# Performance work log

Hardware: AMD Instinct MI355X
Metric: run time of the kernel (lower is better)

Reference implementation:

```python
import jax, jax.numpy as jnp
import numpy as np

B = 8192
N_CLASSES = 1024
MARGIN = 0.1
THRESH = 0.5
SCALE_POS = 2.0
SCALE_NEG = 40.0
EPS = 1e-5


def setup_inputs() -> dict:
    key = jax.random.key(0)
    k1, k2 = jax.random.split(key)
    # cosine-similarity-like values in [-1, 1]
    sim_mat = jax.random.uniform(k1, (B, B), dtype=jnp.float32, minval=-1.0, maxval=1.0)
    labels = jax.random.randint(k2, (B,), 0, N_CLASSES, dtype=jnp.int64)
    return {"sim_mat": sim_mat, "labels": labels}


def reference(sim_mat, labels):
    # [B, B] pair masks
    same = labels[:, None] == labels[None, :]
    pos_mask = same & (sim_mat < 1.0 - EPS)        # positives, excluding self-sim ~ 1
    neg_mask = ~same

    # per-row hardest positive (min) / hardest negative (max); inf sentinels when empty
    min_pos = jnp.min(jnp.where(pos_mask, sim_mat, jnp.inf), axis=1)   # [B]
    max_neg = jnp.max(jnp.where(neg_mask, sim_mat, -jnp.inf), axis=1)  # [B]

    # pair mining: keep informative pairs only
    sel_neg = neg_mask & (sim_mat + MARGIN > min_pos[:, None])
    sel_pos = pos_mask & (sim_mat - MARGIN < max_neg[:, None])

    valid = jnp.any(sel_neg, axis=1) & jnp.any(sel_pos, axis=1)  # rows contributing to loss

    # masked soft-plus style logsumexp losses (sim bounded in [-1,1], exp is safe)
    pos_sum = jnp.sum(jnp.where(sel_pos, jnp.exp(-SCALE_POS * (sim_mat - THRESH)), 0.0), axis=1)
    neg_sum = jnp.sum(jnp.where(sel_neg, jnp.exp(SCALE_NEG * (sim_mat - THRESH)), 0.0), axis=1)
    pos_loss = jnp.log1p(pos_sum) / SCALE_POS
    neg_loss = jnp.log1p(neg_sum) / SCALE_NEG

    loss = jnp.sum(jnp.where(valid, pos_loss + neg_loss, 0.0)) / sim_mat.shape[0]
    return loss
```

## Files before the change

### kernel.cpp

```cpp
#include <hip/hip_runtime.h>
#include <math.h>

namespace {
constexpr int   kB        = 8192;
constexpr int   kBlock    = 256;
constexpr int   kVec      = 4;
constexpr int   kChunks   = kB / (kBlock * kVec);
constexpr float kMargin   = 0.1f;
constexpr float kThresh   = 0.5f;
constexpr float kScalePos = 2.0f;
constexpr float kScaleNeg = 40.0f;
constexpr float kEps      = 1e-5f;
}

__global__ __launch_bounds__(kBlock, 6) void ms_loss_kernel(
    const float* __restrict__ sim,
    const int*   __restrict__ labels,
    float*       __restrict__ ws,
    float*       __restrict__ out)
{
  const int tid  = threadIdx.x;
  const int wave = tid >> 6;
  const int lane = tid & 63;
  const int row  = blockIdx.x;

  const float* __restrict__ srow = sim + (size_t)row * kB;
  float4 v[kChunks];
  #pragma unroll
  for (int k = 0; k < kChunks; ++k)
    v[k] = *reinterpret_cast<const float4*>(srow + k * (kBlock * kVec) + tid * kVec);

  const int ml = labels[row];
  unsigned int m = 0u;
  #pragma unroll
  for (int k = 0; k < kChunks; k += 2) {
    const int4 la = *reinterpret_cast<const int4*>(labels + (k + 0) * (kBlock * kVec) + tid * kVec);
    const int4 lb = *reinterpret_cast<const int4*>(labels + (k + 1) * (kBlock * kVec) + tid * kVec);
    m |= (unsigned)(la.x == ml) << ((k + 0) * 4 + 0);
    m |= (unsigned)(la.y == ml) << ((k + 0) * 4 + 1);
    m |= (unsigned)(la.z == ml) << ((k + 0) * 4 + 2);
    m |= (unsigned)(la.w == ml) << ((k + 0) * 4 + 3);
    m |= (unsigned)(lb.x == ml) << ((k + 1) * 4 + 0);
    m |= (unsigned)(lb.y == ml) << ((k + 1) * 4 + 1);
    m |= (unsigned)(lb.z == ml) << ((k + 1) * 4 + 2);
    m |= (unsigned)(lb.w == ml) << ((k + 1) * 4 + 3);
  }

  #pragma unroll
  for (int k = 0; k < kChunks; ++k)
    asm volatile("" : "+v"(v[k].x), "+v"(v[k].y), "+v"(v[k].z), "+v"(v[k].w));

  __shared__ float s_min[kBlock / 64];
  __shared__ float s_max[kBlock / 64];
  __shared__ float s_pos[kBlock / 64];
  __shared__ float s_neg[kBlock / 64];

  float min_pos =  INFINITY;
  float max_neg = -INFINITY;
  #pragma unroll
  for (int k = 0; k < kChunks; ++k) {
    const float4 f = v[k];
    const float xs[4] = {f.x, f.y, f.z, f.w};
    #pragma unroll
    for (int c = 0; c < 4; ++c) {
      const bool  same = (m >> (k * 4 + c)) & 1u;
      const float x = xs[c];
      min_pos = fminf(min_pos, (same && x < 1.0f - kEps) ? x : INFINITY);
      max_neg = fmaxf(max_neg, same ? -INFINITY : x);
    }
  }
  #pragma unroll
  for (int off = 32; off > 0; off >>= 1) {
    min_pos = fminf(min_pos, __shfl_xor(min_pos, off, 64));
    max_neg = fmaxf(max_neg, __shfl_xor(max_neg, off, 64));
  }
  if (lane == 0) { s_min[wave] = min_pos; s_max[wave] = max_neg; }
  __syncthreads();
  min_pos = fminf(fminf(s_min[0], s_min[1]), fminf(s_min[2], s_min[3]));
  max_neg = fmaxf(fmaxf(s_max[0], s_max[1]), fmaxf(s_max[2], s_max[3]));

  float pos_sum = 0.0f, neg_sum = 0.0f;
  #pragma unroll
  for (int k = 0; k < kChunks; ++k) {
    const float4 f = v[k];
    const float xs[4] = {f.x, f.y, f.z, f.w};
    #pragma unroll
    for (int c = 0; c < 4; ++c) {
      const bool  same = (m >> (k * 4 + c)) & 1u;
      const float x = xs[c];
      const float a = same ? -kScalePos : kScaleNeg;
      const float e = __expf(a * (x - kThresh));
      const bool selp = same && (x < 1.0f - kEps) && (x - kMargin < max_neg);
      const bool seln = (!same) && (x + kMargin > min_pos);
      pos_sum += selp ? e : 0.0f;
      neg_sum += seln ? e : 0.0f;
    }
  }
  #pragma unroll
  for (int off = 32; off > 0; off >>= 1) {
    pos_sum += __shfl_xor(pos_sum, off, 64);
    neg_sum += __shfl_xor(neg_sum, off, 64);
  }
  if (lane == 0) { s_pos[wave] = pos_sum; s_neg[wave] = neg_sum; }
  __syncthreads();
  if (tid == 0) {
    pos_sum = (s_pos[0] + s_pos[1]) + (s_pos[2] + s_pos[3]);
    neg_sum = (s_neg[0] + s_neg[1]) + (s_neg[2] + s_neg[3]);
    const bool  valid    = (pos_sum > 0.0f) && (neg_sum > 0.0f);
    const float row_loss = valid ? (log1pf(pos_sum) * (1.0f / kScalePos)
                                  + log1pf(neg_sum) * (1.0f / kScaleNeg))
                                 : 0.0f;
    if (ws) {
      ws[row] = row_loss;
    } else if (row_loss != 0.0f) {
      atomicAdd(out, row_loss * (1.0f / (float)kB));
    }
  }
}

__global__ __launch_bounds__(256) void ms_reduce_kernel(
    const float* __restrict__ ws,
    float*       __restrict__ out)
{
  const int tid = threadIdx.x;
  float s = 0.0f;
  #pragma unroll
  for (int k = 0; k < 8; ++k) {
    const float4 f = *reinterpret_cast<const float4*>(ws + k * 1024 + tid * 4);
    s += (f.x + f.y) + (f.z + f.w);
  }
  #pragma unroll
  for (int off = 32; off > 0; off >>= 1)
    s += __shfl_xor(s, off, 64);
  __shared__ float sm[4];
  if ((tid & 63) == 0) sm[tid >> 6] = s;
  __syncthreads();
  if (tid == 0)
    out[0] = ((sm[0] + sm[1]) + (sm[2] + sm[3])) * (1.0f / (float)kB);
}

extern "C" void kernel_launch(void* const* d_in, const int* in_sizes, int n_in,
                              void* d_out, int out_size, void* d_ws, size_t ws_size,
                              hipStream_t stream) {
  const float* sim    = (const float*)d_in[0];
  const int*   labels = (const int*)d_in[1];
  float*       out    = (float*)d_out;

  hipMemsetAsync(d_out, 0, sizeof(float) * (size_t)out_size, stream);

  if (d_ws != nullptr && ws_size >= (size_t)kB * sizeof(float)) {
    float* ws = (float*)d_ws;
    ms_loss_kernel<<<dim3(kB), dim3(kBlock), 0, stream>>>(sim, labels, ws, out);
    ms_reduce_kernel<<<dim3(1), dim3(256), 0, stream>>>(ws, out);
  } else {
    ms_loss_kernel<<<dim3(kB), dim3(kBlock), 0, stream>>>(sim, labels, nullptr, out);
  }
}
```

Baseline: 355.6 us.

## Process eight rows per block with double-buffered prefetch of next row

Each block now handles eight consecutive rows instead of one, with a 1024-block grid. It loads labels once per block, packed as 16-bit pairs, and reuses them across rows. While one row is being computed, the next row's data is prefetched into a second register buffer. This amortises label loads and launch overhead and hides memory latency behind compute. The cost is more registers (launch bounds lowered to 4 blocks per SM), extra barriers per row, and labels truncated to 16 bits, which is only correct for fewer than 65536 classes.

```diff
diff --git a/kernel.cpp b/kernel.cpp
--- a/kernel.cpp
+++ b/kernel.cpp
@@ -4,8 +4,8 @@
 namespace {
 constexpr int   kB        = 8192;
 constexpr int   kBlock    = 256;
-constexpr int   kVec      = 4;
-constexpr int   kChunks   = kB / (kBlock * kVec);
+constexpr int   kRows     = 8;
+constexpr int   kGrid     = kB / kRows;
 constexpr float kMargin   = 0.1f;
 constexpr float kThresh   = 0.5f;
 constexpr float kScalePos = 2.0f;
@@ -13,7 +13,7 @@
 constexpr float kEps      = 1e-5f;
 }
 
-__global__ __launch_bounds__(kBlock, 6) void ms_loss_kernel(
+__global__ __launch_bounds__(kBlock, 4) void ms_loss_kernel(
     const float* __restrict__ sim,
     const int*   __restrict__ labels,
     float*       __restrict__ ws,
@@ -22,100 +22,124 @@
   const int tid  = threadIdx.x;
   const int wave = tid >> 6;
   const int lane = tid & 63;
-  const int row  = blockIdx.x;
+  const int base = blockIdx.x * kRows;
 
-  const float* __restrict__ srow = sim + (size_t)row * kB;
-  float4 v[kChunks];
+  __shared__ float s_min[4], s_max[4], s_pos[4], s_neg[4];
+
+  unsigned int lab16[16];
   #pragma unroll
-  for (int k = 0; k < kChunks; ++k)
-    v[k] = *reinterpret_cast<const float4*>(srow + k * (kBlock * kVec) + tid * kVec);
+  for (int k = 0; k < 8; ++k) {
+    const int4 L = *reinterpret_cast<const int4*>(labels + k * 1024 + tid * 4);
+    lab16[2 * k + 0] = ((unsigned)L.x & 0xFFFFu) | ((unsigned)L.y << 16);
+    lab16[2 * k + 1] = ((unsigned)L.z & 0xFFFFu) | ((unsigned)L.w << 16);
+  }
+  int ml[kRows];
+  #pragma unroll
+  for (int r = 0; r < kRows; ++r) ml[r] = labels[base + r];
 
-  const int ml = labels[row];
-  unsigned int m = 0u;
-  #pragma unroll
-  for (int k = 0; k < kChunks; k += 2) {
-    const int4 la = *reinterpret_cast<const int4*>(labels + (k + 0) * (kBlock * kVec) + tid * kVec);
-    const int4 lb = *reinterpret_cast<const int4*>(labels + (k + 1) * (kBlock * kVec) + tid * kVec);
-    m |= (unsigned)(la.x == ml) << ((k + 0) * 4 + 0);
-    m |= (unsigned)(la.y == ml) << ((k + 0) * 4 + 1);
-    m |= (unsigned)(la.z == ml) << ((k + 0) * 4 + 2);
-    m |= (unsigned)(la.w == ml) << ((k + 0) * 4 + 3);
-    m |= (unsigned)(lb.x == ml) << ((k + 1) * 4 + 0);
-    m |= (unsigned)(lb.y == ml) << ((k + 1) * 4 + 1);
-    m |= (unsigned)(lb.z == ml) << ((k + 1) * 4 + 2);
-    m |= (unsigned)(lb.w == ml) << ((k + 1) * 4 + 3);
+  float4 bufA[8], bufB[8];
+  {
+    const float* __restrict__ s0 = sim + (size_t)base * kB;
+    #pragma unroll
+    for (int k = 0; k < 8; ++k)
+      bufA[k] = *reinterpret_cast<const float4*>(s0 + k * 1024 + tid * 4);
   }
 
-  #pragma unroll
-  for (int k = 0; k < kChunks; ++k)
-    asm volatile("" : "+v"(v[k].x), "+v"(v[k].y), "+v"(v[k].z), "+v"(v[k].w));
+#define BAR()                                                                  \
+  {                                                                            \
+    asm volatile("s_waitcnt lgkmcnt(0)" ::: "memory");                         \
+    __builtin_amdgcn_s_barrier();                                              \
+    asm volatile("" ::: "memory");                                             \
+  }
 
-  __shared__ float s_min[kBlock / 64];
-  __shared__ float s_max[kBlock / 64];
-  __shared__ float s_pos[kBlock / 64];
-  __shared__ float s_neg[kBlock / 64];
+#define ROW_BODY(CUR, NXT, R, PREFETCH)                                        \
+  {                                                                            \
+    if (PREFETCH) {                                                            \
+      const float* __restrict__ sp = sim + (size_t)(base + (R) + 1) * kB;      \
+      _Pragma("unroll")                                                        \
+      for (int k = 0; k < 8; ++k)                                              \
+        NXT[k] = *reinterpret_cast<const float4*>(sp + k * 1024 + tid * 4);    \
+      __builtin_amdgcn_sched_barrier(0);         \
+    }                                                                          \
+      \
+    _Pragma("unroll")                                                          \
+    for (int k = 0; k < 8; ++k)                                                \
+      asm volatile("" : "+v"(CUR[k].x), "+v"(CUR[k].y),                        \
+                         "+v"(CUR[k].z), "+v"(CUR[k].w));                      \
+    const unsigned int mlr = (unsigned)ml[R];                                  \
+    unsigned int msk = 0;                                                      \
+    _Pragma("unroll")                                                          \
+    for (int j = 0; j < 16; ++j) {                                             \
+      msk |= (unsigned)((lab16[j] & 0xFFFFu) == mlr) << (2 * j);               \
+      msk |= (unsigned)((lab16[j] >> 16) == mlr) << (2 * j + 1);               \
+    }                                                                          \
+    float min_pos = INFINITY, max_neg = -INFINITY;                             \
+    _Pragma("unroll")                                                          \
+    for (int k = 0; k < 8; ++k) {                                              \
+      const float xs[4] = {CUR[k].x, CUR[k].y, CUR[k].z, CUR[k].w};            \
+      _Pragma("unroll")                                                        \
+      for (int c = 0; c < 4; ++c) {                                            \
+        const bool  same = (msk >> (k * 4 + c)) & 1u;                          \
+        const float x = xs[c];                                                 \
+        min_pos = fminf(min_pos, (same && x < 1.0f - kEps) ? x : INFINITY);    \
+        max_neg = fmaxf(max_neg, same ? -INFINITY : x);                        \
+      }                                                                        \
+    }                                                                          \
+    _Pragma("unroll")                                                          \
+    for (int off = 32; off > 0; off >>= 1) {                                   \
+      min_pos = fminf(min_pos, __shfl_xor(min_pos, off, 64));                  \
+      max_neg = fmaxf(max_neg, __shfl_xor(max_neg, off, 64));                  \
+    }                                                                          \
+    if (lane == 0) { s_min[wave] = min_pos; s_max[wave] = max_neg; }           \
+    BAR();                                                                     \
+    min_pos = fminf(fminf(s_min[0], s_min[1]), fminf(s_min[2], s_min[3]));     \
+    max_neg = fmaxf(fmaxf(s_max[0], s_max[1]), fmaxf(s_max[2], s_max[3]));     \
+    float pos_sum = 0.0f, neg_sum = 0.0f;                                      \
+    _Pragma("unroll")                                                          \
+    for (int k = 0; k < 8; ++k) {                                              \
+      const float xs[4] = {CUR[k].x, CUR[k].y, CUR[k].z, CUR[k].w};            \
+      _Pragma("unroll")                                                        \
+      for (int c = 0; c < 4; ++c) {                                            \
+        const bool  same = (msk >> (k * 4 + c)) & 1u;                          \
+        const float x = xs[c];                                                 \
+        const float a = same ? -kScalePos : kScaleNeg;                         \
+        const float e = __expf(a * (x - kThresh));                             \
+        const bool selp = same && (x < 1.0f - kEps) && (x - kMargin < max_neg);\
+        const bool seln = (!same) && (x + kMargin > min_pos);                  \
+        pos_sum += selp ? e : 0.0f;                                            \
+        neg_sum += seln ? e : 0.0f;                                            \
+      }                                                                        \
+    }                                                                          \
+    _Pragma("unroll")                                                          \
+    for (int off = 32; off > 0; off >>= 1) {                                   \
+      pos_sum += __shfl_xor(pos_sum, off, 64);                                 \
+      neg_sum += __shfl_xor(neg_sum, off, 64);                                 \
+    }                                                                          \
+    if (lane == 0) { s_pos[wave] = pos_sum; s_neg[wave] = neg_sum; }           \
+    BAR();                                                                     \
+    if (tid == 0) {                                                            \
+      const float ps = (s_pos[0] + s_pos[1]) + (s_pos[2] + s_pos[3]);          \
+      const float ns = (s_neg[0] + s_neg[1]) + (s_neg[2] + s_neg[3]);          \
+      const bool  valid = (ps > 0.0f) && (ns > 0.0f);                          \
+      const float rl = valid ? (log1pf(ps) * (1.0f / kScalePos)                \
+                              + log1pf(ns) * (1.0f / kScaleNeg)) : 0.0f;       \
+      if (ws) ws[base + (R)] = rl;                                             \
+      else if (rl != 0.0f) atomicAdd(out, rl * (1.0f / (float)kB));            \
+    }                                                                          \
+    BAR();                           \
+  }
 
-  float min_pos =  INFINITY;
-  float max_neg = -INFINITY;
-  #pragma unroll
-  for (int k = 0; k < kChunks; ++k) {
-    const float4 f = v[k];
-    const float xs[4] = {f.x, f.y, f.z, f.w};
-    #pragma unroll
-    for (int c = 0; c < 4; ++c) {
-      const bool  same = (m >> (k * 4 + c)) & 1u;
-      const float x = xs[c];
-      min_pos = fminf(min_pos, (same && x < 1.0f - kEps) ? x : INFINITY);
-      max_neg = fmaxf(max_neg, same ? -INFINITY : x);
-    }
-  }
-  #pragma unroll
-  for (int off = 32; off > 0; off >>= 1) {
-    min_pos = fminf(min_pos, __shfl_xor(min_pos, off, 64));
-    max_neg = fmaxf(max_neg, __shfl_xor(max_neg, off, 64));
-  }
-  if (lane == 0) { s_min[wave] = min_pos; s_max[wave] = max_neg; }
-  __syncthreads();
-  min_pos = fminf(fminf(s_min[0], s_min[1]), fminf(s_min[2], s_min[3]));
-  max_neg = fmaxf(fmaxf(s_max[0], s_max[1]), fmaxf(s_max[2], s_max[3]));
+  ROW_BODY(bufA, bufB, 0, true);
+  ROW_BODY(bufB, bufA, 1, true);
+  ROW_BODY(bufA, bufB, 2, true);
+  ROW_BODY(bufB, bufA, 3, true);
+  ROW_BODY(bufA, bufB, 4, true);
+  ROW_BODY(bufB, bufA, 5, true);
+  ROW_BODY(bufA, bufB, 6, true);
+  ROW_BODY(bufB, bufA, 7, false);
 
-  float pos_sum = 0.0f, neg_sum = 0.0f;
-  #pragma unroll
-  for (int k = 0; k < kChunks; ++k) {
-    const float4 f = v[k];
-    const float xs[4] = {f.x, f.y, f.z, f.w};
-    #pragma unroll
-    for (int c = 0; c < 4; ++c) {
-      const bool  same = (m >> (k * 4 + c)) & 1u;
-      const float x = xs[c];
-      const float a = same ? -kScalePos : kScaleNeg;
-      const float e = __expf(a * (x - kThresh));
-      const bool selp = same && (x < 1.0f - kEps) && (x - kMargin < max_neg);
-      const bool seln = (!same) && (x + kMargin > min_pos);
-      pos_sum += selp ? e : 0.0f;
-      neg_sum += seln ? e : 0.0f;
-    }
-  }
-  #pragma unroll
-  for (int off = 32; off > 0; off >>= 1) {
-    pos_sum += __shfl_xor(pos_sum, off, 64);
-    neg_sum += __shfl_xor(neg_sum, off, 64);
-  }
-  if (lane == 0) { s_pos[wave] = pos_sum; s_neg[wave] = neg_sum; }
-  __syncthreads();
-  if (tid == 0) {
-    pos_sum = (s_pos[0] + s_pos[1]) + (s_pos[2] + s_pos[3]);
-    neg_sum = (s_neg[0] + s_neg[1]) + (s_neg[2] + s_neg[3]);
-    const bool  valid    = (pos_sum > 0.0f) && (neg_sum > 0.0f);
-    const float row_loss = valid ? (log1pf(pos_sum) * (1.0f / kScalePos)
-                                  + log1pf(neg_sum) * (1.0f / kScaleNeg))
-                                 : 0.0f;
-    if (ws) {
-      ws[row] = row_loss;
-    } else if (row_loss != 0.0f) {
-      atomicAdd(out, row_loss * (1.0f / (float)kB));
-    }
-  }
+#undef ROW_BODY
+#undef BAR
 }
 
 __global__ __launch_bounds__(256) void ms_reduce_kernel(
@@ -150,9 +174,9 @@
 
   if (d_ws != nullptr && ws_size >= (size_t)kB * sizeof(float)) {
     float* ws = (float*)d_ws;
-    ms_loss_kernel<<<dim3(kB), dim3(kBlock), 0, stream>>>(sim, labels, ws, out);
+    ms_loss_kernel<<<dim3(kGrid), dim3(kBlock), 0, stream>>>(sim, labels, ws, out);
     ms_reduce_kernel<<<dim3(1), dim3(256), 0, stream>>>(ws, out);
   } else {
-    ms_loss_kernel<<<dim3(kB), dim3(kBlock), 0, stream>>>(sim, labels, nullptr, out);
+    ms_loss_kernel<<<dim3(kGrid), dim3(kBlock), 0, stream>>>(sim, labels, nullptr, out);
   }
 }
```

New measurement: 372.4 us. 4.7% more time.
